# Performance work log

Measured on AMD Instinct MI355X. Metric: run time of the kernel, lower is better.

Reference implementation:

```python
import jax, jax.numpy as jnp
import numpy as np

HEADS = 8
HEAD_DIM = 64
SCALE = HEAD_DIM ** -0.5


def setup_inputs() -> dict:
    key = jax.random.key(0)
    ks = jax.random.split(key, 5)
    d_model, inner = 1024, HEADS * HEAD_DIM  # 512
    x = jax.random.normal(ks[0], (2, 2048, d_model), dtype=jnp.float32)
    # torch Linear weights stored pre-transposed as [in, out]
    Wq = jax.random.normal(ks[1], (d_model, inner), dtype=jnp.float32) * (d_model ** -0.5)
    Wkv = jax.random.normal(ks[2], (d_model, 2 * inner), dtype=jnp.float32) * (d_model ** -0.5)
    Wo = jax.random.normal(ks[3], (inner, d_model), dtype=jnp.float32) * (inner ** -0.5)
    bo = jnp.zeros((d_model,), dtype=jnp.float32)
    return {"x": x, "Wq": Wq, "Wkv": Wkv, "Wo": Wo, "bo": bo}


def reference(x, Wq, Wkv, Wo, bo):
    b, n, _ = x.shape
    q = x @ Wq                       # [b, n, h*d]
    kv = x @ Wkv                     # [b, n, 2*h*d] (self-attention: context = x)
    k, v = jnp.split(kv, 2, axis=-1)

    def split_heads(t):
        return t.reshape(b, n, HEADS, HEAD_DIM).transpose(0, 2, 1, 3)  # [b, h, n, d]

    q, k, v = map(split_heads, (q, k, v))
    sim = jnp.einsum('bhid,bhjd->bhij', q, k) * SCALE  # [b, h, n, n]
    attn = jax.nn.softmax(sim, axis=-1)                # dropout p=0.0 -> identity
    out = jnp.einsum('bhij,bhjd->bhid', attn, v)       # [b, h, n, d]
    out = out.transpose(0, 2, 1, 3).reshape(b, n, HEADS * HEAD_DIM)
    return out @ Wo + bo
```

## Files before the change

kernel.cpp:

```cpp
#include <hip/hip_runtime.h>

typedef _Float16 f16;
typedef __attribute__((ext_vector_type(4))) _Float16 f16x4;
typedef __attribute__((ext_vector_type(8))) _Float16 f16x8;
typedef __attribute__((ext_vector_type(4))) float f32x4;

#define CEXP 0.18033688011112042f
#define QKB_LD 1056
#define VTB_LD 2080

__device__ __forceinline__ void gload16(const f16* g, f16* l) {
    __builtin_amdgcn_global_load_lds((const __attribute__((address_space(1))) void*)g,
                                     (__attribute__((address_space(3))) void*)l, 16, 0, 0);
}

__global__ __launch_bounds__(256) void conv_f32_f16_k(const float* __restrict__ in,
                                                      f16* __restrict__ out) {
    int idx = (blockIdx.x * 256 + threadIdx.x) * 8;
    float4 a = *(const float4*)(in + idx);
    float4 b = *(const float4*)(in + idx + 4);
    f16x8 o;
    o[0] = (f16)a.x; o[1] = (f16)a.y; o[2] = (f16)a.z; o[3] = (f16)a.w;
    o[4] = (f16)b.x; o[5] = (f16)b.y; o[6] = (f16)b.z; o[7] = (f16)b.w;
    *(f16x8*)(out + idx) = o;
}

__global__ __launch_bounds__(256) void transpose_conv_k(const float* __restrict__ in,
                                                        f16* __restrict__ out,
                                                        int N, int ldo, int row_off) {
    __shared__ float tile[32][33];
    int tx = threadIdx.x & 31, ty = threadIdx.x >> 5;
    int n0 = blockIdx.x * 32, k0 = blockIdx.y * 32;
#pragma unroll
    for (int j = 0; j < 4; j++)
        tile[ty + j * 8][tx] = in[(size_t)(k0 + ty + j * 8) * N + n0 + tx];
    __syncthreads();
#pragma unroll
    for (int j = 0; j < 4; j++)
        out[(size_t)(row_off + n0 + ty + j * 8) * ldo + k0 + tx] = (f16)tile[tx][ty + j * 8];
}

template <int MODE>
__global__ __launch_bounds__(256) void gemm128_k(
    const f16* __restrict__ A, const f16* __restrict__ Bt,
    f16* __restrict__ Cqk, f16* __restrict__ Cvt,
    float* __restrict__ Cout, const float* __restrict__ bias,
    int K, int NTILES) {
    __shared__ __align__(16) f16 As[128 * 72];
    __shared__ __align__(16) f16 Bs[128 * 72];
    int bid = blockIdx.x;
    int nt = bid % NTILES, mt = bid / NTILES;
    int m0 = mt * 128, n0 = nt * 128;
    int tid = threadIdx.x;
    int lane = tid & 63, w = tid >> 6;
    int wm = w >> 1, wn = w & 1;
    int lr = lane & 15, lg = lane >> 4;
    f32x4 acc[4][4] = {};

    for (int k0 = 0; k0 < K; k0 += 64) {
#pragma unroll
        for (int i = 0; i < 4; i++) {
            int c = tid + i * 256;
            int row = c >> 3, kc = c & 7;
            uint4 va = *(const uint4*)(A + (size_t)(m0 + row) * K + k0 + kc * 8);
            uint4 vb = *(const uint4*)(Bt + (size_t)(n0 + row) * K + k0 + kc * 8);
            *(uint4*)(&As[row * 72 + kc * 8]) = va;
            *(uint4*)(&Bs[row * 72 + kc * 8]) = vb;
        }
        __syncthreads();
#pragma unroll
        for (int ks = 0; ks < 2; ks++) {
            f16x8 af[4], bf[4];
#pragma unroll
            for (int i = 0; i < 4; i++)
                af[i] = *(const f16x8*)(&As[(wm * 64 + i * 16 + lr) * 72 + ks * 32 + lg * 8]);
#pragma unroll
            for (int j = 0; j < 4; j++)
                bf[j] = *(const f16x8*)(&Bs[(wn * 64 + j * 16 + lr) * 72 + ks * 32 + lg * 8]);
#pragma unroll
            for (int i = 0; i < 4; i++)
#pragma unroll
                for (int j = 0; j < 4; j++)
                    acc[i][j] = __builtin_amdgcn_mfma_f32_16x16x32_f16(af[i], bf[j], acc[i][j], 0, 0, 0);
        }
        __syncthreads();
    }

#pragma unroll
    for (int i = 0; i < 4; i++) {
#pragma unroll
        for (int j = 0; j < 4; j++) {
            int row = m0 + wm * 64 + i * 16 + lg * 4;
            int col = n0 + wn * 64 + j * 16 + lr;
            if (MODE == 1) {
                float bv = bias[col];
#pragma unroll
                for (int r = 0; r < 4; r++)
                    Cout[(size_t)(row + r) * 1024 + col] = acc[i][j][r] + bv;
            } else {
                if (col < 1024) {
#pragma unroll
                    for (int r = 0; r < 4; r++)
                        Cqk[(size_t)(row + r) * QKB_LD + col] = (f16)acc[i][j][r];
                } else {
                    int c = col - 1024;
                    int hh = c >> 6, d = c & 63;
                    int bb = row >> 11, n = row & 2047;
                    f16x4 ov;
#pragma unroll
                    for (int r = 0; r < 4; r++) ov[r] = (f16)acc[i][j][r];
                    *(f16x4*)(Cvt + (size_t)((bb * 8 + hh) * 64 + d) * VTB_LD + n) = ov;
                }
            }
        }
    }
}

__global__ __launch_bounds__(256, 2) void attn_k(const f16* __restrict__ qkb,
                                                 const f16* __restrict__ vt,
                                                 f16* __restrict__ ao) {
    __shared__ __align__(16) f16 Ks[2][128 * 64];
    __shared__ __align__(16) f16 Vs[2][64 * 128];

    int bid = blockIdx.x;
    int xcd = bid & 7;
    int pair = xcd * 2 + ((bid >> 3) & 1);
    int qblk = bid >> 4;
    int b = pair >> 3, h = pair & 7;
    int tid = threadIdx.x;
    int lane = tid & 63, w = tid >> 6;
    int lr = lane & 15, lg = lane >> 4;
    int q0 = qblk * 64 + w * 16;

    const f16* qb = qkb + (size_t)b * 2048 * QKB_LD + h * 64;
    const f16* kb = qb + 512;
    const f16* vb = vt + (size_t)pair * 64 * VTB_LD;

    f16x8 qf0 = *(const f16x8*)(qb + (size_t)(q0 + lr) * QKB_LD + lg * 8);
    f16x8 qf1 = *(const f16x8*)(qb + (size_t)(q0 + lr) * QKB_LD + 32 + lg * 8);

    int kColSrc = ((lane & 7) * 8) ^ ((lane >> 3) << 3);
    int kRowL = (lane >> 3);
    int vColSrc = ((lane & 15) * 8) ^ ((lane >> 4) << 3);
    int vRowL = (lane >> 4);

    int kOffA = (lg * 8) ^ ((lr & 7) << 3);
    int vOffL = (lg * 4) ^ ((lr & 7) << 3);

    {
        const f16* ksrc = kb + (size_t)(w * 32 + kRowL) * QKB_LD + kColSrc;
        const f16* vsrc = vb + (size_t)(w * 16 + vRowL) * VTB_LD + vColSrc;
#pragma unroll
        for (int j = 0; j < 4; j++) {
            gload16(ksrc + (size_t)j * 8 * QKB_LD, &Ks[0][(w * 32 + j * 8) * 64]);
            gload16(vsrc + (size_t)(j * 4) * VTB_LD + ((j & 1) << 5) - (((j & 1) << 5) & vColSrc) * 2,
                    &Vs[0][(w * 16 + j * 4) * 128]);
        }
    }
    __syncthreads();

    f32x4 acc[4] = {};
    float m = -INFINITY, l = 0.f;

    for (int t = 0; t < 16; t++) {
        int cur = t & 1;
        if (t < 15) {
            int kv1 = (t + 1) * 128;
            int nxt = cur ^ 1;
            const f16* ksrc = kb + (size_t)(kv1 + w * 32 + kRowL) * QKB_LD + kColSrc;
            const f16* vsrc0 = vb + (size_t)(w * 16 + vRowL) * VTB_LD + kv1;
#pragma unroll
            for (int j = 0; j < 4; j++) {
                gload16(ksrc + (size_t)j * 8 * QKB_LD, &Ks[nxt][(w * 32 + j * 8) * 64]);
                gload16(vsrc0 + (size_t)(j * 4) * VTB_LD + (vColSrc ^ ((j & 1) << 5)),
                        &Vs[nxt][(w * 16 + j * 4) * 128]);
            }
        }

        f32x4 s[8];
        __builtin_amdgcn_s_setprio(1);
#pragma unroll
        for (int kg = 0; kg < 8; kg++) {
            const f16* krow = &Ks[cur][(kg * 16 + lr) * 64];
            f16x8 ka0 = *(const f16x8*)(krow + kOffA);
            f16x8 ka1 = *(const f16x8*)(krow + (kOffA ^ 32));
            f32x4 z = {};
            z = __builtin_amdgcn_mfma_f32_16x16x32_f16(ka0, qf0, z, 0, 0, 0);
            s[kg] = __builtin_amdgcn_mfma_f32_16x16x32_f16(ka1, qf1, z, 0, 0, 0);
        }
        __builtin_amdgcn_s_setprio(0);

        float mx = -INFINITY;
#pragma unroll
        for (int kg = 0; kg < 8; kg++)
#pragma unroll
            for (int r = 0; r < 4; r++)
                mx = fmaxf(mx, s[kg][r]);
        mx = fmaxf(mx, __shfl_xor(mx, 16, 64));
        mx = fmaxf(mx, __shfl_xor(mx, 32, 64));
        float mn = fmaxf(m, mx);
        float alpha = __builtin_amdgcn_exp2f((m - mn) * CEXP);
        m = mn;
        float rs = 0.f;
        f16x4 pf[8];
#pragma unroll
        for (int kg = 0; kg < 8; kg++)
#pragma unroll
            for (int r = 0; r < 4; r++) {
                float p = __builtin_amdgcn_exp2f((s[kg][r] - mn) * CEXP);
                rs += p;
                pf[kg][r] = (f16)p;
            }
        rs += __shfl_xor(rs, 16, 64);
        rs += __shfl_xor(rs, 32, 64);
        l = l * alpha + rs;
#pragma unroll
        for (int dg = 0; dg < 4; dg++)
#pragma unroll
            for (int r = 0; r < 4; r++)
                acc[dg][r] *= alpha;

        __builtin_amdgcn_s_setprio(1);
#pragma unroll
        for (int kg = 0; kg < 8; kg++)
#pragma unroll
            for (int dg = 0; dg < 4; dg++) {
                f16x4 vf = *(const f16x4*)(&Vs[cur][(dg * 16 + lr) * 128 + (vOffL ^ (kg << 4))]);
                acc[dg] = __builtin_amdgcn_mfma_f32_16x16x16f16(vf, pf[kg], acc[dg], 0, 0, 0);
            }
        __builtin_amdgcn_s_setprio(0);

        __syncthreads();
    }

    float inv = 1.f / l;
#pragma unroll
    for (int dg = 0; dg < 4; dg++) {
        f16x4 ov;
#pragma unroll
        for (int r = 0; r < 4; r++) ov[r] = (f16)(acc[dg][r] * inv);
        *(f16x4*)(ao + (size_t)(b * 2048 + q0 + lr) * 512 + h * 64 + dg * 16 + lg * 4) = ov;
    }
}

extern "C" void kernel_launch(void* const* d_in, const int* in_sizes, int n_in,
                              void* d_out, int out_size, void* d_ws, size_t ws_size,
                              hipStream_t stream) {
    const float* x   = (const float*)d_in[0];
    const float* Wq  = (const float*)d_in[1];
    const float* Wkv = (const float*)d_in[2];
    const float* Wo  = (const float*)d_in[3];
    const float* bo  = (const float*)d_in[4];
    float* out = (float*)d_out;

    f16* xb    = (f16*)d_ws;
    f16* wqkvT = xb + 4096 * 1024;
    f16* woT   = wqkvT + 1536 * 1024;
    f16* qkb   = woT + 1024 * 512;
    f16* vtb   = qkb + 4096 * QKB_LD;
    f16* ao    = vtb + 16 * 64 * VTB_LD;

    conv_f32_f16_k<<<2048, 256, 0, stream>>>(x, xb);
    transpose_conv_k<<<dim3(16, 32), 256, 0, stream>>>(Wq, wqkvT, 512, 1024, 0);
    transpose_conv_k<<<dim3(32, 32), 256, 0, stream>>>(Wkv, wqkvT, 1024, 1024, 512);
    transpose_conv_k<<<dim3(32, 16), 256, 0, stream>>>(Wo, woT, 1024, 512, 0);

    gemm128_k<0><<<32 * 12, 256, 0, stream>>>(xb, wqkvT, qkb, vtb, nullptr, nullptr, 1024, 12);
    attn_k<<<512, 256, 0, stream>>>(qkb, vtb, ao);
    gemm128_k<1><<<32 * 8, 256, 0, stream>>>(ao, woT, nullptr, nullptr, out, bo, 512, 8);
}
```

Measured before the change: 94.70 us.

## Halve attention KV tile, raise occupancy, lazy rescale, fold softmax scale into Q

The attention KV tile shrinks from 128 to 64 keys, halving LDS use so four blocks per CU can be resident instead of two, with a new XOR swizzle for the V tile. The QKV GEMM now pre-multiplies Q by the softmax-scale constant, which removes the per-element multiply in the exp2 path. Online softmax rescaling is skipped unless the running max grows by more than 8 (in log2 units). The GEMM's global-to-LDS copies also switch to direct global_load_lds with an unpadded layout. In exchange there are twice as many loop iterations and barriers, and the unpadded GEMM LDS layout may cause bank conflicts.

```diff
diff --git a/kernel.cpp b/kernel.cpp
--- a/kernel.cpp
+++ b/kernel.cpp
@@ -46,8 +46,8 @@
     f16* __restrict__ Cqk, f16* __restrict__ Cvt,
     float* __restrict__ Cout, const float* __restrict__ bias,
     int K, int NTILES) {
-    __shared__ __align__(16) f16 As[128 * 72];
-    __shared__ __align__(16) f16 Bs[128 * 72];
+    __shared__ __align__(16) f16 As[128 * 64];
+    __shared__ __align__(16) f16 Bs[128 * 64];
     int bid = blockIdx.x;
     int nt = bid % NTILES, mt = bid / NTILES;
     int m0 = mt * 128, n0 = nt * 128;
@@ -55,17 +55,17 @@
     int lane = tid & 63, w = tid >> 6;
     int wm = w >> 1, wn = w & 1;
     int lr = lane & 15, lg = lane >> 4;
+    int rowL = lane >> 3;
+    int colL = (lane & 7) * 8;
+    const f16* aSrc = A + (size_t)(m0 + w * 32 + rowL) * K + colL;
+    const f16* bSrc = Bt + (size_t)(n0 + w * 32 + rowL) * K + colL;
     f32x4 acc[4][4] = {};
 
     for (int k0 = 0; k0 < K; k0 += 64) {
 #pragma unroll
-        for (int i = 0; i < 4; i++) {
-            int c = tid + i * 256;
-            int row = c >> 3, kc = c & 7;
-            uint4 va = *(const uint4*)(A + (size_t)(m0 + row) * K + k0 + kc * 8);
-            uint4 vb = *(const uint4*)(Bt + (size_t)(n0 + row) * K + k0 + kc * 8);
-            *(uint4*)(&As[row * 72 + kc * 8]) = va;
-            *(uint4*)(&Bs[row * 72 + kc * 8]) = vb;
+        for (int j = 0; j < 4; j++) {
+            gload16(aSrc + k0 + (size_t)(j * 8) * K, &As[(w * 32 + j * 8) * 64]);
+            gload16(bSrc + k0 + (size_t)(j * 8) * K, &Bs[(w * 32 + j * 8) * 64]);
         }
         __syncthreads();
 #pragma unroll
@@ -73,10 +73,10 @@
             f16x8 af[4], bf[4];
 #pragma unroll
             for (int i = 0; i < 4; i++)
-                af[i] = *(const f16x8*)(&As[(wm * 64 + i * 16 + lr) * 72 + ks * 32 + lg * 8]);
+                af[i] = *(const f16x8*)(&As[(wm * 64 + i * 16 + lr) * 64 + ks * 32 + lg * 8]);
 #pragma unroll
             for (int j = 0; j < 4; j++)
-                bf[j] = *(const f16x8*)(&Bs[(wn * 64 + j * 16 + lr) * 72 + ks * 32 + lg * 8]);
+                bf[j] = *(const f16x8*)(&Bs[(wn * 64 + j * 16 + lr) * 64 + ks * 32 + lg * 8]);
 #pragma unroll
             for (int i = 0; i < 4; i++)
 #pragma unroll
@@ -99,9 +99,10 @@
                     Cout[(size_t)(row + r) * 1024 + col] = acc[i][j][r] + bv;
             } else {
                 if (col < 1024) {
+                    float sc = (col < 512) ? CEXP : 1.0f;
 #pragma unroll
                     for (int r = 0; r < 4; r++)
-                        Cqk[(size_t)(row + r) * QKB_LD + col] = (f16)acc[i][j][r];
+                        Cqk[(size_t)(row + r) * QKB_LD + col] = (f16)(acc[i][j][r] * sc);
                 } else {
                     int c = col - 1024;
                     int hh = c >> 6, d = c & 63;
@@ -116,11 +117,11 @@
     }
 }
 
-__global__ __launch_bounds__(256, 2) void attn_k(const f16* __restrict__ qkb,
+__global__ __launch_bounds__(256, 4) void attn_k(const f16* __restrict__ qkb,
                                                  const f16* __restrict__ vt,
                                                  f16* __restrict__ ao) {
-    __shared__ __align__(16) f16 Ks[2][128 * 64];
-    __shared__ __align__(16) f16 Vs[2][64 * 128];
+    __shared__ __align__(16) f16 Ks[2][64 * 64];
+    __shared__ __align__(16) f16 Vs[2][64 * 64];
 
     int bid = blockIdx.x;
     int xcd = bid & 7;
@@ -139,48 +140,40 @@
     f16x8 qf0 = *(const f16x8*)(qb + (size_t)(q0 + lr) * QKB_LD + lg * 8);
     f16x8 qf1 = *(const f16x8*)(qb + (size_t)(q0 + lr) * QKB_LD + 32 + lg * 8);
 
-    int kColSrc = ((lane & 7) * 8) ^ ((lane >> 3) << 3);
-    int kRowL = (lane >> 3);
-    int vColSrc = ((lane & 15) * 8) ^ ((lane >> 4) << 3);
-    int vRowL = (lane >> 4);
+    int srcCol = (((lane & 7) ^ (lane >> 3)) << 3);
+    int rowL = lane >> 3;
+    const f16* ksrc = kb + (size_t)(w * 16 + rowL) * QKB_LD + srcCol;
+    const f16* vsrc = vb + (size_t)(w * 16 + rowL) * VTB_LD + srcCol;
+
+#pragma unroll
+    for (int j = 0; j < 2; j++) {
+        gload16(ksrc + (size_t)(j * 8) * QKB_LD, &Ks[0][(w * 16 + j * 8) * 64]);
+        gload16(vsrc + (size_t)(j * 8) * VTB_LD, &Vs[0][(w * 16 + j * 8) * 64]);
+    }
+    __syncthreads();
 
     int kOffA = (lg * 8) ^ ((lr & 7) << 3);
-    int vOffL = (lg * 4) ^ ((lr & 7) << 3);
-
-    {
-        const f16* ksrc = kb + (size_t)(w * 32 + kRowL) * QKB_LD + kColSrc;
-        const f16* vsrc = vb + (size_t)(w * 16 + vRowL) * VTB_LD + vColSrc;
-#pragma unroll
-        for (int j = 0; j < 4; j++) {
-            gload16(ksrc + (size_t)j * 8 * QKB_LD, &Ks[0][(w * 32 + j * 8) * 64]);
-            gload16(vsrc + (size_t)(j * 4) * VTB_LD + ((j & 1) << 5) - (((j & 1) << 5) & vColSrc) * 2,
-                    &Vs[0][(w * 16 + j * 4) * 128]);
-        }
-    }
-    __syncthreads();
+    int lr7 = lr & 7;
 
     f32x4 acc[4] = {};
     float m = -INFINITY, l = 0.f;
 
-    for (int t = 0; t < 16; t++) {
+    for (int t = 0; t < 32; t++) {
         int cur = t & 1;
-        if (t < 15) {
-            int kv1 = (t + 1) * 128;
+        if (t < 31) {
+            int kv1 = (t + 1) * 64;
             int nxt = cur ^ 1;
-            const f16* ksrc = kb + (size_t)(kv1 + w * 32 + kRowL) * QKB_LD + kColSrc;
-            const f16* vsrc0 = vb + (size_t)(w * 16 + vRowL) * VTB_LD + kv1;
-#pragma unroll
-            for (int j = 0; j < 4; j++) {
-                gload16(ksrc + (size_t)j * 8 * QKB_LD, &Ks[nxt][(w * 32 + j * 8) * 64]);
-                gload16(vsrc0 + (size_t)(j * 4) * VTB_LD + (vColSrc ^ ((j & 1) << 5)),
-                        &Vs[nxt][(w * 16 + j * 4) * 128]);
-            }
-        }
-
-        f32x4 s[8];
+#pragma unroll
+            for (int j = 0; j < 2; j++) {
+                gload16(ksrc + (size_t)(kv1 + j * 8) * QKB_LD, &Ks[nxt][(w * 16 + j * 8) * 64]);
+                gload16(vsrc + (size_t)(j * 8) * VTB_LD + kv1, &Vs[nxt][(w * 16 + j * 8) * 64]);
+            }
+        }
+
+        f32x4 s[4];
         __builtin_amdgcn_s_setprio(1);
 #pragma unroll
-        for (int kg = 0; kg < 8; kg++) {
+        for (int kg = 0; kg < 4; kg++) {
             const f16* krow = &Ks[cur][(kg * 16 + lr) * 64];
             f16x8 ka0 = *(const f16x8*)(krow + kOffA);
             f16x8 ka1 = *(const f16x8*)(krow + (kOffA ^ 32));
@@ -192,40 +185,44 @@
 
         float mx = -INFINITY;
 #pragma unroll
-        for (int kg = 0; kg < 8; kg++)
+        for (int kg = 0; kg < 4; kg++)
 #pragma unroll
             for (int r = 0; r < 4; r++)
                 mx = fmaxf(mx, s[kg][r]);
         mx = fmaxf(mx, __shfl_xor(mx, 16, 64));
         mx = fmaxf(mx, __shfl_xor(mx, 32, 64));
-        float mn = fmaxf(m, mx);
-        float alpha = __builtin_amdgcn_exp2f((m - mn) * CEXP);
-        m = mn;
+        if (!__all(mx - m <= 8.f)) {
+            float mn = fmaxf(m, mx);
+            float alpha = __builtin_amdgcn_exp2f(m - mn);
+            m = mn;
+            l *= alpha;
+#pragma unroll
+            for (int dg = 0; dg < 4; dg++)
+#pragma unroll
+                for (int r = 0; r < 4; r++)
+                    acc[dg][r] *= alpha;
+        }
         float rs = 0.f;
-        f16x4 pf[8];
-#pragma unroll
-        for (int kg = 0; kg < 8; kg++)
+        f16x4 pf[4];
+#pragma unroll
+        for (int kg = 0; kg < 4; kg++)
 #pragma unroll
             for (int r = 0; r < 4; r++) {
-                float p = __builtin_amdgcn_exp2f((s[kg][r] - mn) * CEXP);
+                float p = __builtin_amdgcn_exp2f(s[kg][r] - m);
                 rs += p;
                 pf[kg][r] = (f16)p;
             }
         rs += __shfl_xor(rs, 16, 64);
         rs += __shfl_xor(rs, 32, 64);
-        l = l * alpha + rs;
-#pragma unroll
-        for (int dg = 0; dg < 4; dg++)
-#pragma unroll
-            for (int r = 0; r < 4; r++)
-                acc[dg][r] *= alpha;
+        l += rs;
 
         __builtin_amdgcn_s_setprio(1);
 #pragma unroll
-        for (int kg = 0; kg < 8; kg++)
+        for (int kg = 0; kg < 4; kg++)
 #pragma unroll
             for (int dg = 0; dg < 4; dg++) {
-                f16x4 vf = *(const f16x4*)(&Vs[cur][(dg * 16 + lr) * 128 + (vOffL ^ (kg << 4))]);
+                int vpe = (((kg * 2 + (lg >> 1)) ^ lr7) << 3) + (lg & 1) * 4;
+                f16x4 vf = *(const f16x4*)(&Vs[cur][(dg * 16 + lr) * 64 + vpe]);
                 acc[dg] = __builtin_amdgcn_mfma_f32_16x16x16f16(vf, pf[kg], acc[dg], 0, 0, 0);
             }
         __builtin_amdgcn_s_setprio(0);
```

Measured after the change: 109.2 us. 1.15x slower.
